# Kernel tuning notes

Measured on AMD Instinct MI355X. Metric: run time of the kernel, lower is better.

Reference implementation:

```python
import jax, jax.numpy as jnp
import numpy as np

N = 50000
IN_DIM = 256
HID = 64
HEADS = 4
OUT_DIM = 64
E = 800000
SLOPE = 0.2


def gat_conv(x, src, dst, W, a_src, a_dst, bias, heads, out_ch):
    """PyG-style GATConv: gather -> edge attention -> segment softmax -> scatter.
    x: [N, in], W: [in, heads*out_ch], a_src/a_dst: [heads, out_ch], bias: [heads*out_ch].
    Returns [N, heads*out_ch] (heads concatenated)."""
    n = x.shape[0]
    h = (x @ W).reshape(n, heads, out_ch)               # [N, H, C]
    s = jnp.einsum('nhc,hc->nh', h, a_src)              # [N, H]
    d = jnp.einsum('nhc,hc->nh', h, a_dst)              # [N, H]
    e = jax.nn.leaky_relu(s[src] + d[dst], SLOPE)       # [E, H]
    emax = jax.ops.segment_max(e, dst, num_segments=n)  # stable softmax per dst
    ex = jnp.exp(e - emax[dst])
    denom = jax.ops.segment_sum(ex, dst, num_segments=n)
    alpha = ex / (denom[dst] + 1e-16)                   # [E, H]
    msg = h[src] * alpha[:, :, None]                    # [E, H, C]
    out = jax.ops.segment_sum(msg, dst, num_segments=n) # [N, H, C]
    return out.reshape(n, heads * out_ch) + bias


def setup_inputs() -> dict:
    key = jax.random.key(0)
    ks = jax.random.split(key, 12)
    x = jax.random.normal(ks[0], (N, IN_DIM), dtype=jnp.float32)
    edge_index = jax.random.randint(ks[1], (2, E), 0, N, dtype=jnp.int64)
    sc = 0.1
    params = {
        'W1': jax.random.normal(ks[2], (IN_DIM, HEADS * HID), dtype=jnp.float32) * sc,
        'a_src1': jax.random.normal(ks[3], (HEADS, HID), dtype=jnp.float32) * sc,
        'a_dst1': jax.random.normal(ks[4], (HEADS, HID), dtype=jnp.float32) * sc,
        'b1': jnp.zeros((HEADS * HID,), dtype=jnp.float32),
        'W2': jax.random.normal(ks[5], (HEADS * HID, HID), dtype=jnp.float32) * sc,
        'a_src2': jax.random.normal(ks[6], (1, HID), dtype=jnp.float32) * sc,
        'a_dst2': jax.random.normal(ks[7], (1, HID), dtype=jnp.float32) * sc,
        'b2': jnp.zeros((HID,), dtype=jnp.float32),
        'Wf1': jax.random.normal(ks[8], (HID, HID), dtype=jnp.float32) * sc,
        'bf1': jnp.zeros((HID,), dtype=jnp.float32),
        'Wf2': jax.random.normal(ks[9], (HID, OUT_DIM), dtype=jnp.float32) * sc,
        'bf2': jnp.zeros((OUT_DIM,), dtype=jnp.float32),
    }
    return {'x': x, 'edge_index': edge_index, **params}


def reference(x, edge_index, W1, a_src1, a_dst1, b1, W2, a_src2, a_dst2, b2,
              Wf1, bf1, Wf2, bf2):
    n = x.shape[0]
    # PyG GATConv adds self-loops by default
    loops = jnp.arange(n, dtype=edge_index.dtype)
    src = jnp.concatenate([edge_index[0], loops])
    dst = jnp.concatenate([edge_index[1], loops])
    h = jax.nn.relu(gat_conv(x, src, dst, W1, a_src1, a_dst1, b1, HEADS, HID))
    h = jax.nn.relu(gat_conv(h, src, dst, W2, a_src2, a_dst2, b2, 1, HID))
    h = jax.nn.relu(h @ Wf1 + bf1)
    return jax.nn.softmax(h @ Wf2 + bf2, axis=1)
```

## Files before the change

### kernel.cpp

```cpp
#include <hip/hip_runtime.h>

#define NNODES 50000
#define NEDGES 800000
#define INDIM  256
#define HIDC   64
#define HEADS  4
static constexpr int ETOT = NEDGES + NNODES;

typedef _Float16 half8 __attribute__((ext_vector_type(8)));
typedef short    s16x8 __attribute__((ext_vector_type(8)));
typedef short    s16x4 __attribute__((ext_vector_type(4)));
typedef float    f32x4 __attribute__((ext_vector_type(4)));

__device__ __forceinline__ unsigned short f2bf(float f) {
    unsigned u = __float_as_uint(f);
    u += 0x7fffu + ((u >> 16) & 1u);
    return (unsigned short)(u >> 16);
}
__device__ __forceinline__ float bf2f(unsigned short h) {
    return __uint_as_float(((unsigned)h) << 16);
}

__device__ __forceinline__ int is_int64(const unsigned* __restrict__ ei32) {
    int r = 1;
    #pragma unroll
    for (int i = 1; i < 64; i += 2) r &= (ei32[i] == 0u);
    return r;
}

__device__ __forceinline__ int load_idx(const void* ei, int is64, size_t pos) {
    return is64 ? (int)((const long long*)ei)[pos] : ((const int*)ei)[pos];
}

__global__ __launch_bounds__(256)
void hist_k(const void* __restrict__ ei, int* __restrict__ count) {
    int e = blockIdx.x * 256 + threadIdx.x;
    if (e >= ETOT) return;
    int is64 = is_int64((const unsigned*)ei);
    int dst = (e < NEDGES) ? load_idx(ei, is64, (size_t)NEDGES + e) : (e - NEDGES);
    atomicAdd(&count[dst], 1);
}

__global__ __launch_bounds__(1024)
void scan1_k(const int* __restrict__ count, int* __restrict__ rowptr,
             int* __restrict__ bsum, int n) {
    __shared__ int wsum[16];
    const int tid = threadIdx.x;
    const int lane = tid & 63;
    const int w = tid >> 6;
    int i = blockIdx.x * 1024 + tid;
    int v = (i < n) ? count[i] : 0;
    int x = v;
    #pragma unroll
    for (int dd = 1; dd < 64; dd <<= 1) {
        int y = __shfl_up(x, dd);
        if (lane >= dd) x += y;
    }
    if (lane == 63) wsum[w] = x;
    __syncthreads();
    int woff = 0, total = 0;
    #pragma unroll
    for (int j = 0; j < 16; ++j) {
        if (j < w) woff += wsum[j];
        total += wsum[j];
    }
    if (i < n) rowptr[i] = woff + x - v;
    if (tid == 0) bsum[blockIdx.x] = total;
}

__global__ void scan2_k(int* __restrict__ bsum, int* __restrict__ bpre, int nb,
                        int* __restrict__ rowptr, int n) {
    int lane = threadIdx.x;
    int v = (lane < nb) ? bsum[lane] : 0;
    int x = v;
    #pragma unroll
    for (int dd = 1; dd < 64; dd <<= 1) {
        int y = __shfl_up(x, dd);
        if (lane >= dd) x += y;
    }
    if (lane < nb) bpre[lane] = x - v;
    if (lane == 63) rowptr[n] = x;
}

__global__ __launch_bounds__(1024)
void scan3_k(int* __restrict__ rowptr, const int* __restrict__ bpre, int n) {
    int i = blockIdx.x * 1024 + threadIdx.x;
    if (i < n) rowptr[i] += bpre[blockIdx.x];
}

__global__ __launch_bounds__(256)
void scatter_k(const void* __restrict__ ei, const int* __restrict__ rowptr,
               int* __restrict__ fill, int* __restrict__ csr_src) {
    int e = blockIdx.x * 256 + threadIdx.x;
    if (e >= ETOT) return;
    int is64 = is_int64((const unsigned*)ei);
    int src, dst;
    if (e < NEDGES) {
        src = load_idx(ei, is64, (size_t)e);
        dst = load_idx(ei, is64, (size_t)NEDGES + e);
    } else {
        src = e - NEDGES; dst = src;
    }
    int pos = rowptr[dst] + atomicAdd(&fill[dst], 1);
    csr_src[pos] = src;
}

__global__ __launch_bounds__(256)
void convall_k(const float* __restrict__ W1, const float* __restrict__ W2,
               const float* __restrict__ Wf1, const float* __restrict__ Wf2,
               unsigned short* __restrict__ w1h, unsigned short* __restrict__ w1l,
               unsigned short* __restrict__ w2h, unsigned short* __restrict__ w2l,
               unsigned short* __restrict__ f1h, unsigned short* __restrict__ f1l,
               unsigned short* __restrict__ f2h, unsigned short* __restrict__ f2l) {
    int idx = blockIdx.x * 256 + threadIdx.x;
    const float* W; unsigned short *th, *tl; int K, N;
    if (idx < 65536)       { W = W1;  th = w1h; tl = w1l; K = 256; N = 256; }
    else if (idx < 81920)  { idx -= 65536; W = W2;  th = w2h; tl = w2l; K = 256; N = 64; }
    else if (idx < 86016)  { idx -= 81920; W = Wf1; th = f1h; tl = f1l; K = 64;  N = 64; }
    else if (idx < 90112)  { idx -= 86016; W = Wf2; th = f2h; tl = f2l; K = 64;  N = 64; }
    else return;
    int k = idx / N, n = idx % N;
    float w = W[(size_t)k * N + n];
    unsigned short hi = f2bf(w);
    unsigned short lo = f2bf(w - bf2f(hi));
    th[(size_t)n * K + k] = hi;
    tl[(size_t)n * K + k] = lo;
}

template<int BN, int SD>
__global__ __launch_bounds__(256)
void gemm_mfma_k(const float* __restrict__ A,
                 const unsigned short* __restrict__ Bt_hi,
                 const unsigned short* __restrict__ Bt_lo,
                 _Float16* __restrict__ Ch,
                 const float* __restrict__ asrc, const float* __restrict__ adst,
                 float* __restrict__ S, float* __restrict__ D,
                 int M, int N, int K) {
    constexpr int CB = BN / 32;
    constexpr int BI = (BN * 4) / 256;
    __shared__ unsigned short sAh[128][40], sAl[128][40];
    __shared__ unsigned short sBh[BN][40], sBl[BN][40];
    const int tid = threadIdx.x;
    const int bm = blockIdx.y * 128;
    const int bn = blockIdx.x * BN;
    const int w = tid >> 6, lane = tid & 63;
    const int wr = w >> 1, wc = w & 1;
    const int lr = lane & 15, lk = lane >> 4;

    f32x4 acc[4][CB] = {};

    for (int k0 = 0; k0 < K; k0 += 32) {
        float4 av[4];
        #pragma unroll
        for (int i = 0; i < 4; ++i) {
            int idx = tid + 256 * i;
            int row = idx >> 3, c4 = idx & 7;
            int grow = bm + row; if (grow >= M) grow = M - 1;
            av[i] = *(const float4*)(A + (size_t)grow * K + k0 + c4 * 4);
        }
        s16x8 bhv[BI], blv[BI];
        #pragma unroll
        for (int i = 0; i < BI; ++i) {
            int idx = tid + 256 * i;
            int col = idx >> 2, ch = idx & 3;
            bhv[i] = *(const s16x8*)(Bt_hi + (size_t)(bn + col) * K + k0 + ch * 8);
            blv[i] = *(const s16x8*)(Bt_lo + (size_t)(bn + col) * K + k0 + ch * 8);
        }
        __syncthreads();
        #pragma unroll
        for (int i = 0; i < 4; ++i) {
            int idx = tid + 256 * i;
            int row = idx >> 3, c4 = idx & 7;
            float vs[4] = {av[i].x, av[i].y, av[i].z, av[i].w};
            unsigned short h[4], l[4];
            #pragma unroll
            for (int j = 0; j < 4; ++j) {
                h[j] = f2bf(vs[j]);
                l[j] = f2bf(vs[j] - bf2f(h[j]));
            }
            *(s16x4*)&sAh[row][c4 * 4] = (s16x4){(short)h[0], (short)h[1], (short)h[2], (short)h[3]};
            *(s16x4*)&sAl[row][c4 * 4] = (s16x4){(short)l[0], (short)l[1], (short)l[2], (short)l[3]};
        }
        #pragma unroll
        for (int i = 0; i < BI; ++i) {
            int idx = tid + 256 * i;
            int col = idx >> 2, ch = idx & 3;
            *(s16x8*)&sBh[col][ch * 8] = bhv[i];
            *(s16x8*)&sBl[col][ch * 8] = blv[i];
        }
        __syncthreads();
        s16x8 afh[4], afl[4], bfh[CB], bfl[CB];
        #pragma unroll
        for (int rb = 0; rb < 4; ++rb) {
            int row = wr * 64 + rb * 16 + lr;
            afh[rb] = *(const s16x8*)&sAh[row][lk * 8];
            afl[rb] = *(const s16x8*)&sAl[row][lk * 8];
        }
        #pragma unroll
        for (int cb = 0; cb < CB; ++cb) {
            int col = wc * (BN / 2) + cb * 16 + lr;
            bfh[cb] = *(const s16x8*)&sBh[col][lk * 8];
            bfl[cb] = *(const s16x8*)&sBl[col][lk * 8];
        }
        #pragma unroll
        for (int rb = 0; rb < 4; ++rb)
            #pragma unroll
            for (int cb = 0; cb < CB; ++cb) {
                acc[rb][cb] = __builtin_amdgcn_mfma_f32_16x16x32_bf16(afh[rb], bfh[cb], acc[rb][cb], 0, 0, 0);
                acc[rb][cb] = __builtin_amdgcn_mfma_f32_16x16x32_bf16(afh[rb], bfl[cb], acc[rb][cb], 0, 0, 0);
                acc[rb][cb] = __builtin_amdgcn_mfma_f32_16x16x32_bf16(afl[rb], bfh[cb], acc[rb][cb], 0, 0, 0);
            }
    }
    #pragma unroll
    for (int rb = 0; rb < 4; ++rb)
        #pragma unroll
        for (int cb = 0; cb < CB; ++cb)
            #pragma unroll
            for (int r = 0; r < 4; ++r) {
                int row = bm + wr * 64 + rb * 16 + lk * 4 + r;
                int col = bn + wc * (BN / 2) + cb * 16 + lr;
                if (row < M) Ch[(size_t)row * N + col] = (_Float16)acc[rb][cb][r];
            }
    {
        float af[CB], df[CB];
        #pragma unroll
        for (int cb = 0; cb < CB; ++cb) {
            int colg = bn + wc * (BN / 2) + cb * 16 + lr;
            af[cb] = asrc[colg];
            df[cb] = adst[colg];
        }
        #pragma unroll
        for (int rb = 0; rb < 4; ++rb)
            #pragma unroll
            for (int r = 0; r < 4; ++r) {
                float ps = 0.f, pd = 0.f;
                #pragma unroll
                for (int cb = 0; cb < CB; ++cb) {
                    ps += acc[rb][cb][r] * af[cb];
                    pd += acc[rb][cb][r] * df[cb];
                }
                #pragma unroll
                for (int m = 1; m < 16; m <<= 1) {
                    ps += __shfl_xor(ps, m);
                    pd += __shfl_xor(pd, m);
                }
                int row = bm + wr * 64 + rb * 16 + lk * 4 + r;
                if (lr == 0 && row < M) {
                    if constexpr (SD == 1) {
                        int head = (bn + wc * (BN / 2)) >> 6;
                        S[(size_t)row * (N >> 6) + head] = ps;
                        D[(size_t)row * (N >> 6) + head] = pd;
                    } else {
                        atomicAdd(&S[row], ps);
                        atomicAdd(&D[row], pd);
                    }
                }
            }
    }
}

__device__ __forceinline__ float leaky(float e) { return (e > 0.f) ? e : 0.2f * e; }

__device__ __forceinline__ float sel4(const float v[4], int idx) {
    float r = v[0];
    r = (idx == 1) ? v[1] : r;
    r = (idx == 2) ? v[2] : r;
    r = (idx == 3) ? v[3] : r;
    return r;
}

template<int H>
__global__ __launch_bounds__(256)
void agg_k(const _Float16* __restrict__ hhalf,
           const float* __restrict__ s, const float* __restrict__ d,
           const float* __restrict__ bias, const int* __restrict__ rowptr,
           const int* __restrict__ csr_src, float* __restrict__ out, int n) {
    __shared__ float exs[4][H][64];
    __shared__ int   srcs[4][64];
    const int lane = threadIdx.x & 63;
    const int wv   = threadIdx.x >> 6;
    const int node = blockIdx.x * 4 + wv;
    if (node >= n) return;
    const int beg = rowptr[node], end = rowptr[node + 1];
    float dh[H], dn[H];
    #pragma unroll
    for (int h = 0; h < H; ++h) { dh[h] = d[node * H + h]; dn[h] = 0.f; }
    const half8* H8 = (const half8*)hhalf;

    if constexpr (H == 4) {
        const int sub = lane >> 5, c8 = lane & 31, head = c8 >> 3;
        float acc[8] = {};
        for (int c0 = beg; c0 < end; c0 += 64) {
            const int cend = (c0 + 64 < end) ? c0 + 64 : end;
            int e = c0 + lane;
            if (e < end) {
                int sidx = csr_src[e];
                float4 sv = *(const float4*)(s + (size_t)sidx * 4);
                float e0 = __expf(leaky(sv.x + dh[0]));
                float e1 = __expf(leaky(sv.y + dh[1]));
                float e2 = __expf(leaky(sv.z + dh[2]));
                float e3 = __expf(leaky(sv.w + dh[3]));
                srcs[wv][lane] = sidx;
                exs[wv][0][lane] = e0; exs[wv][1][lane] = e1;
                exs[wv][2][lane] = e2; exs[wv][3][lane] = e3;
                dn[0] += e0; dn[1] += e1; dn[2] += e2; dn[3] += e3;
            }
            asm volatile("s_waitcnt lgkmcnt(0)" ::: "memory");
            int i = c0;
            for (; i + 7 < cend; i += 8) {
                int j = i - c0 + sub;
                int s0 = srcs[wv][j],     s1 = srcs[wv][j + 2];
                int s2 = srcs[wv][j + 4], s3 = srcs[wv][j + 6];
                float x0 = exs[wv][head][j],     x1 = exs[wv][head][j + 2];
                float x2 = exs[wv][head][j + 4], x3 = exs[wv][head][j + 6];
                half8 h0 = H8[(size_t)s0 * 32 + c8];
                half8 h1 = H8[(size_t)s1 * 32 + c8];
                half8 h2 = H8[(size_t)s2 * 32 + c8];
                half8 h3 = H8[(size_t)s3 * 32 + c8];
                #pragma unroll
                for (int q = 0; q < 8; ++q)
                    acc[q] += x0 * (float)h0[q] + x1 * (float)h1[q]
                            + x2 * (float)h2[q] + x3 * (float)h3[q];
            }
            for (; i < cend; i += 2) {
                int e2i = i + sub;
                if (e2i < cend) {
                    int j = e2i - c0;
                    int s0 = srcs[wv][j];
                    float x = exs[wv][head][j];
                    half8 hh = H8[(size_t)s0 * 32 + c8];
                    #pragma unroll
                    for (int q = 0; q < 8; ++q) acc[q] += x * (float)hh[q];
                }
            }
        }
        float inv_[4];
        #pragma unroll
        for (int h = 0; h < 4; ++h) {
            #pragma unroll
            for (int m = 32; m; m >>= 1) dn[h] += __shfl_xor(dn[h], m);
            inv_[h] = 1.f / (dn[h] + 1e-16f);
        }
        const float invh = sel4(inv_, head);
        #pragma unroll
        for (int q = 0; q < 8; ++q) acc[q] += __shfl_xor(acc[q], 32);
        if (lane < 32) {
            float4 b0 = *(const float4*)(bias + c8 * 8);
            float4 b1 = *(const float4*)(bias + c8 * 8 + 4);
            float4 o0, o1;
            o0.x = fmaxf(acc[0] * invh + b0.x, 0.f);
            o0.y = fmaxf(acc[1] * invh + b0.y, 0.f);
            o0.z = fmaxf(acc[2] * invh + b0.z, 0.f);
            o0.w = fmaxf(acc[3] * invh + b0.w, 0.f);
            o1.x = fmaxf(acc[4] * invh + b1.x, 0.f);
            o1.y = fmaxf(acc[5] * invh + b1.y, 0.f);
            o1.z = fmaxf(acc[6] * invh + b1.z, 0.f);
            o1.w = fmaxf(acc[7] * invh + b1.w, 0.f);
            *(float4*)(out + (size_t)node * 256 + c8 * 8) = o0;
            *(float4*)(out + (size_t)node * 256 + c8 * 8 + 4) = o1;
        }
    } else {
        const int sub = lane >> 3, c8 = lane & 7;
        float acc[8] = {};
        for (int c0 = beg; c0 < end; c0 += 64) {
            const int cend = (c0 + 64 < end) ? c0 + 64 : end;
            int e = c0 + lane;
            if (e < end) {
                int sidx = csr_src[e];
                float ex = __expf(leaky(s[sidx] + dh[0]));
                srcs[wv][lane] = sidx;
                exs[wv][0][lane] = ex;
                dn[0] += ex;
            }
            asm volatile("s_waitcnt lgkmcnt(0)" ::: "memory");
            int i = c0;
            for (; i + 15 < cend; i += 16) {
                int j = i - c0 + sub;
                int s0 = srcs[wv][j], s1 = srcs[wv][j + 8];
                float x0 = exs[wv][0][j], x1 = exs[wv][0][j + 8];
                half8 h0 = H8[(size_t)s0 * 8 + c8];
                half8 h1 = H8[(size_t)s1 * 8 + c8];
                #pragma unroll
                for (int q = 0; q < 8; ++q)
                    acc[q] += x0 * (float)h0[q] + x1 * (float)h1[q];
            }
            for (; i < cend; i += 8) {
                int e2i = i + sub;
                if (e2i < cend) {
                    int j = e2i - c0;
                    int s0 = srcs[wv][j];
                    float x = exs[wv][0][j];
                    half8 hh = H8[(size_t)s0 * 8 + c8];
                    #pragma unroll
                    for (int q = 0; q < 8; ++q) acc[q] += x * (float)hh[q];
                }
            }
        }
        #pragma unroll
        for (int m = 32; m; m >>= 1) dn[0] += __shfl_xor(dn[0], m);
        const float inv0 = 1.f / (dn[0] + 1e-16f);
        #pragma unroll
        for (int m = 8; m <= 32; m <<= 1)
            #pragma unroll
            for (int q = 0; q < 8; ++q) acc[q] += __shfl_xor(acc[q], m);
        if (lane < 8) {
            float4 b0 = *(const float4*)(bias + c8 * 8);
            float4 b1 = *(const float4*)(bias + c8 * 8 + 4);
            float4 o0, o1;
            o0.x = fmaxf(acc[0] * inv0 + b0.x, 0.f);
            o0.y = fmaxf(acc[1] * inv0 + b0.y, 0.f);
            o0.z = fmaxf(acc[2] * inv0 + b0.z, 0.f);
            o0.w = fmaxf(acc[3] * inv0 + b0.w, 0.f);
            o1.x = fmaxf(acc[4] * inv0 + b1.x, 0.f);
            o1.y = fmaxf(acc[5] * inv0 + b1.y, 0.f);
            o1.z = fmaxf(acc[6] * inv0 + b1.z, 0.f);
            o1.w = fmaxf(acc[7] * inv0 + b1.w, 0.f);
            *(float4*)(out + (size_t)node * 64 + c8 * 8) = o0;
            *(float4*)(out + (size_t)node * 64 + c8 * 8 + 4) = o1;
        }
    }
}

__global__ __launch_bounds__(256)
void ffm_k(const float* __restrict__ in,
           const unsigned short* __restrict__ w1h, const unsigned short* __restrict__ w1l,
           const float* __restrict__ bf1,
           const unsigned short* __restrict__ w2h, const unsigned short* __restrict__ w2l,
           const float* __restrict__ bf2, float* __restrict__ out, int M) {
    __shared__ unsigned short sAh[64][80], sAl[64][80];
    __shared__ unsigned short sW1h[64][80], sW1l[64][80];
    __shared__ unsigned short sW2h[64][80], sW2l[64][80];
    const int tid = threadIdx.x;
    const int bm = blockIdx.x * 64;
    const int w = tid >> 6, lane = tid & 63;
    const int lr = lane & 15, lk = lane >> 4;

    for (int c = tid; c < 512; c += 256) {
        int n = c >> 3, k8 = c & 7;
        int dcol = (k8 >> 2) * 40 + (k8 & 3) * 8;
        *(s16x8*)&sW1h[n][dcol] = *(const s16x8*)(w1h + n * 64 + k8 * 8);
        *(s16x8*)&sW1l[n][dcol] = *(const s16x8*)(w1l + n * 64 + k8 * 8);
        *(s16x8*)&sW2h[n][dcol] = *(const s16x8*)(w2h + n * 64 + k8 * 8);
        *(s16x8*)&sW2l[n][dcol] = *(const s16x8*)(w2l + n * 64 + k8 * 8);
    }
    #pragma unroll
    for (int i = 0; i < 4; ++i) {
        int c = tid + 256 * i;
        int row = c >> 4, c4 = c & 15;
        int grow = bm + row; if (grow >= M) grow = M - 1;
        float4 av = *(const float4*)(in + (size_t)grow * 64 + c4 * 4);
        float vs[4] = {av.x, av.y, av.z, av.w};
        unsigned short h[4], l[4];
        #pragma unroll
        for (int j = 0; j < 4; ++j) {
            h[j] = f2bf(vs[j]);
            l[j] = f2bf(vs[j] - bf2f(h[j]));
        }
        int dcol = (c4 >> 3) * 40 + (c4 & 7) * 4;
        *(s16x4*)&sAh[row][dcol] = (s16x4){(short)h[0], (short)h[1], (short)h[2], (short)h[3]};
        *(s16x4*)&sAl[row][dcol] = (s16x4){(short)l[0], (short)l[1], (short)l[2], (short)l[3]};
    }
    __syncthreads();
    f32x4 a1[4] = {};
    #pragma unroll
    for (int ks = 0; ks < 2; ++ks) {
        int koff = ks * 40 + lk * 8;
        s16x8 ah = *(const s16x8*)&sAh[w * 16 + lr][koff];
        s16x8 al = *(const s16x8*)&sAl[w * 16 + lr][koff];
        #pragma unroll
        for (int cb = 0; cb < 4; ++cb) {
            s16x8 bh = *(const s16x8*)&sW1h[cb * 16 + lr][koff];
            s16x8 bl = *(const s16x8*)&sW1l[cb * 16 + lr][koff];
            a1[cb] = __builtin_amdgcn_mfma_f32_16x16x32_bf16(ah, bh, a1[cb], 0, 0, 0);
            a1[cb] = __builtin_amdgcn_mfma_f32_16x16x32_bf16(ah, bl, a1[cb], 0, 0, 0);
            a1[cb] = __builtin_amdgcn_mfma_f32_16x16x32_bf16(al, bh, a1[cb], 0, 0, 0);
        }
    }
    __syncthreads();
    #pragma unroll
    for (int cb = 0; cb < 4; ++cb) {
        int col = cb * 16 + lr;
        float b = bf1[col];
        int dcol = (col >> 5) * 40 + (col & 31);
        #pragma unroll
        for (int r = 0; r < 4; ++r) {
            int row = w * 16 + lk * 4 + r;
            float y = fmaxf(a1[cb][r] + b, 0.f);
            unsigned short hh = f2bf(y);
            sAh[row][dcol] = hh;
            sAl[row][dcol] = f2bf(y - bf2f(hh));
        }
    }
    __syncthreads();
    f32x4 a2[4] = {};
    #pragma unroll
    for (int ks = 0; ks < 2; ++ks) {
        int koff = ks * 40 + lk * 8;
        s16x8 ah = *(const s16x8*)&sAh[w * 16 + lr][koff];
        s16x8 al = *(const s16x8*)&sAl[w * 16 + lr][koff];
        #pragma unroll
        for (int cb = 0; cb < 4; ++cb) {
            s16x8 bh = *(const s16x8*)&sW2h[cb * 16 + lr][koff];
            s16x8 bl = *(const s16x8*)&sW2l[cb * 16 + lr][koff];
            a2[cb] = __builtin_amdgcn_mfma_f32_16x16x32_bf16(ah, bh, a2[cb], 0, 0, 0);
            a2[cb] = __builtin_amdgcn_mfma_f32_16x16x32_bf16(ah, bl, a2[cb], 0, 0, 0);
            a2[cb] = __builtin_amdgcn_mfma_f32_16x16x32_bf16(al, bh, a2[cb], 0, 0, 0);
        }
    }
    float zb[4];
    #pragma unroll
    for (int cb = 0; cb < 4; ++cb) zb[cb] = bf2[cb * 16 + lr];
    #pragma unroll
    for (int r = 0; r < 4; ++r) {
        int row = bm + w * 16 + lk * 4 + r;
        float z0 = a2[0][r] + zb[0], z1 = a2[1][r] + zb[1];
        float z2 = a2[2][r] + zb[2], z3 = a2[3][r] + zb[3];
        float m = fmaxf(fmaxf(z0, z1), fmaxf(z2, z3));
        #pragma unroll
        for (int dd = 1; dd < 16; dd <<= 1) m = fmaxf(m, __shfl_xor(m, dd));
        float e0 = __expf(z0 - m), e1 = __expf(z1 - m);
        float e2 = __expf(z2 - m), e3 = __expf(z3 - m);
        float sum = e0 + e1 + e2 + e3;
        #pragma unroll
        for (int dd = 1; dd < 16; dd <<= 1) sum += __shfl_xor(sum, dd);
        float is = 1.f / sum;
        if (row < M) {
            out[(size_t)row * 64 + 0 + lr]  = e0 * is;
            out[(size_t)row * 64 + 16 + lr] = e1 * is;
            out[(size_t)row * 64 + 32 + lr] = e2 * is;
            out[(size_t)row * 64 + 48 + lr] = e3 * is;
        }
    }
}

extern "C" void kernel_launch(void* const* d_in, const int* in_sizes, int n_in,
                              void* d_out, int out_size, void* d_ws, size_t ws_size,
                              hipStream_t stream) {
    const float* x      = (const float*)d_in[0];
    const void*  ei     = d_in[1];
    const float* W1     = (const float*)d_in[2];
    const float* a_src1 = (const float*)d_in[3];
    const float* a_dst1 = (const float*)d_in[4];
    const float* b1     = (const float*)d_in[5];
    const float* W2     = (const float*)d_in[6];
    const float* a_src2 = (const float*)d_in[7];
    const float* a_dst2 = (const float*)d_in[8];
    const float* b2     = (const float*)d_in[9];
    const float* Wf1    = (const float*)d_in[10];
    const float* bf1    = (const float*)d_in[11];
    const float* Wf2    = (const float*)d_in[12];
    const float* bf2    = (const float*)d_in[13];
    float* outp = (float*)d_out;

    char* ws = (char*)d_ws;
    size_t off = 0;
    auto take = [&](size_t bytes) -> char* {
        char* p = ws + off;
        off += (bytes + 255) & ~(size_t)255;
        return p;
    };
    int*   count  = (int*)take((size_t)NNODES * 4);
    int*   fill   = (int*)take((size_t)NNODES * 4);
    int*   rowptr = (int*)take((size_t)(NNODES + 1) * 4);
    int*   bsum   = (int*)take(64 * 4);
    int*   bpre   = (int*)take(64 * 4);
    int*   csr    = (int*)take((size_t)ETOT * 4);
    unsigned short* w1t_hi = (unsigned short*)take((size_t)256 * 256 * 2);
    unsigned short* w1t_lo = (unsigned short*)take((size_t)256 * 256 * 2);
    unsigned short* w2t_hi = (unsigned short*)take((size_t)64 * 256 * 2);
    unsigned short* w2t_lo = (unsigned short*)take((size_t)64 * 256 * 2);
    unsigned short* wf1t_hi = (unsigned short*)take((size_t)64 * 64 * 2);
    unsigned short* wf1t_lo = (unsigned short*)take((size_t)64 * 64 * 2);
    unsigned short* wf2t_hi = (unsigned short*)take((size_t)64 * 64 * 2);
    unsigned short* wf2t_lo = (unsigned short*)take((size_t)64 * 64 * 2);
    float* agg1   = (float*)take((size_t)NNODES * 256 * 4);
    float* s1     = (float*)take((size_t)NNODES * HEADS * 4);
    float* d1     = (float*)take((size_t)NNODES * HEADS * 4);
    _Float16* h1h = (_Float16*)take((size_t)NNODES * 256 * 2);
    float*    s2   = s1;
    float*    d2   = d1;
    float*    agg2 = agg1;
    _Float16* h2h  = h1h;

    hipMemsetAsync(count, 0, (size_t)((char*)fill - (char*)count) + (size_t)NNODES * 4, stream);
    const int eblocks = (ETOT + 255) / 256;
    hist_k<<<eblocks, 256, 0, stream>>>(ei, count);
    const int sblocks = (NNODES + 1023) / 1024;
    scan1_k<<<sblocks, 1024, 0, stream>>>(count, rowptr, bsum, NNODES);
    scan2_k<<<1, 64, 0, stream>>>(bsum, bpre, sblocks, rowptr, NNODES);
    scan3_k<<<sblocks, 1024, 0, stream>>>(rowptr, bpre, NNODES);
    scatter_k<<<eblocks, 256, 0, stream>>>(ei, rowptr, fill, csr);

    convall_k<<<(90112 + 255) / 256, 256, 0, stream>>>(
        W1, W2, Wf1, Wf2, w1t_hi, w1t_lo, w2t_hi, w2t_lo,
        wf1t_hi, wf1t_lo, wf2t_hi, wf2t_lo);

    const int nodeblocks = NNODES / 4;
    const int mblocks = (NNODES + 127) / 128;
    const dim3 gg1(2, mblocks);
    const dim3 gg2(1, mblocks);

    gemm_mfma_k<128, 1><<<gg1, 256, 0, stream>>>(x, w1t_hi, w1t_lo,
        h1h, a_src1, a_dst1, s1, d1, NNODES, 256, 256);
    agg_k<HEADS><<<nodeblocks, 256, 0, stream>>>(h1h, s1, d1, b1,
        rowptr, csr, agg1, NNODES);

    hipMemsetAsync(s2, 0, (size_t)((char*)d1 - (char*)s1) + (size_t)NNODES * 4, stream);
    gemm_mfma_k<64, 2><<<gg2, 256, 0, stream>>>(agg1, w2t_hi, w2t_lo,
        h2h, a_src2, a_dst2, s2, d2, NNODES, 64, 256);
    agg_k<1><<<nodeblocks, 256, 0, stream>>>(h2h, s2, d2, b2,
        rowptr, csr, agg2, NNODES);

    ffm_k<<<(NNODES + 63) / 64, 256, 0, stream>>>(agg2, wf1t_hi, wf1t_lo,
        bf1, wf2t_hi, wf2t_lo, bf2, outp, NNODES);
}
```

Before: 280.3 us.

## Store layer-1 aggregate in fp16, merge scan kernels, drop atomics for layer-2 scores

The layer-1 aggregation now writes its ReLU output as fp16 instead of fp32, and the second GEMM is templated to read fp16 A directly, which halves that intermediate's write and read traffic. The two scan tail kernels are merged into one that recomputes block prefixes per block with wave reductions. Layer-2 attention scores are combined across the two column warps through shared memory and written directly, which removes the atomics and the memset before them. The fp16 intermediate adds rounding error on the hidden activations.

```diff
diff --git a/kernel.cpp b/kernel.cpp
--- a/kernel.cpp
+++ b/kernel.cpp
@@ -68,24 +68,25 @@
     if (tid == 0) bsum[blockIdx.x] = total;
 }
 
-__global__ void scan2_k(int* __restrict__ bsum, int* __restrict__ bpre, int nb,
-                        int* __restrict__ rowptr, int n) {
-    int lane = threadIdx.x;
-    int v = (lane < nb) ? bsum[lane] : 0;
-    int x = v;
-    #pragma unroll
-    for (int dd = 1; dd < 64; dd <<= 1) {
-        int y = __shfl_up(x, dd);
-        if (lane >= dd) x += y;
-    }
-    if (lane < nb) bpre[lane] = x - v;
-    if (lane == 63) rowptr[n] = x;
-}
-
 __global__ __launch_bounds__(1024)
-void scan3_k(int* __restrict__ rowptr, const int* __restrict__ bpre, int n) {
-    int i = blockIdx.x * 1024 + threadIdx.x;
-    if (i < n) rowptr[i] += bpre[blockIdx.x];
+void scan3_k(int* __restrict__ rowptr, const int* __restrict__ bsum,
+             int nb, int n) {
+    __shared__ int spre, stot;
+    const int tid = threadIdx.x;
+    if (tid < 64) {
+        int vall = (tid < nb) ? bsum[tid] : 0;
+        int vpre = (tid < (int)blockIdx.x) ? vall : 0;
+        #pragma unroll
+        for (int m = 32; m; m >>= 1) {
+            vall += __shfl_xor(vall, m);
+            vpre += __shfl_xor(vpre, m);
+        }
+        if (tid == 0) { spre = vpre; stot = vall; }
+    }
+    __syncthreads();
+    int i = blockIdx.x * 1024 + tid;
+    if (i < n) rowptr[i] += spre;
+    if (blockIdx.x == 0 && tid == 0) rowptr[n] = stot;
 }
 
 __global__ __launch_bounds__(256)
@@ -127,9 +128,9 @@
     tl[(size_t)n * K + k] = lo;
 }
 
-template<int BN, int SD>
+template<int BN, int SD, typename AT>
 __global__ __launch_bounds__(256)
-void gemm_mfma_k(const float* __restrict__ A,
+void gemm_mfma_k(const AT* __restrict__ A,
                  const unsigned short* __restrict__ Bt_hi,
                  const unsigned short* __restrict__ Bt_lo,
                  _Float16* __restrict__ Ch,
@@ -151,12 +152,23 @@
 
     for (int k0 = 0; k0 < K; k0 += 32) {
         float4 av[4];
-        #pragma unroll
-        for (int i = 0; i < 4; ++i) {
-            int idx = tid + 256 * i;
-            int row = idx >> 3, c4 = idx & 7;
-            int grow = bm + row; if (grow >= M) grow = M - 1;
-            av[i] = *(const float4*)(A + (size_t)grow * K + k0 + c4 * 4);
+        half8 avh[2];
+        if constexpr (sizeof(AT) == 4) {
+            #pragma unroll
+            for (int i = 0; i < 4; ++i) {
+                int idx = tid + 256 * i;
+                int row = idx >> 3, c4 = idx & 7;
+                int grow = bm + row; if (grow >= M) grow = M - 1;
+                av[i] = *(const float4*)((const float*)A + (size_t)grow * K + k0 + c4 * 4);
+            }
+        } else {
+            #pragma unroll
+            for (int i = 0; i < 2; ++i) {
+                int idx = tid + 256 * i;
+                int row = idx >> 2, c8 = idx & 3;
+                int grow = bm + row; if (grow >= M) grow = M - 1;
+                avh[i] = *(const half8*)((const _Float16*)A + (size_t)grow * K + k0 + c8 * 8);
+            }
         }
         s16x8 bhv[BI], blv[BI];
         #pragma unroll
@@ -167,19 +179,38 @@
             blv[i] = *(const s16x8*)(Bt_lo + (size_t)(bn + col) * K + k0 + ch * 8);
         }
         __syncthreads();
-        #pragma unroll
-        for (int i = 0; i < 4; ++i) {
-            int idx = tid + 256 * i;
-            int row = idx >> 3, c4 = idx & 7;
-            float vs[4] = {av[i].x, av[i].y, av[i].z, av[i].w};
-            unsigned short h[4], l[4];
-            #pragma unroll
-            for (int j = 0; j < 4; ++j) {
-                h[j] = f2bf(vs[j]);
-                l[j] = f2bf(vs[j] - bf2f(h[j]));
-            }
-            *(s16x4*)&sAh[row][c4 * 4] = (s16x4){(short)h[0], (short)h[1], (short)h[2], (short)h[3]};
-            *(s16x4*)&sAl[row][c4 * 4] = (s16x4){(short)l[0], (short)l[1], (short)l[2], (short)l[3]};
+        if constexpr (sizeof(AT) == 4) {
+            #pragma unroll
+            for (int i = 0; i < 4; ++i) {
+                int idx = tid + 256 * i;
+                int row = idx >> 3, c4 = idx & 7;
+                float vs[4] = {av[i].x, av[i].y, av[i].z, av[i].w};
+                unsigned short h[4], l[4];
+                #pragma unroll
+                for (int j = 0; j < 4; ++j) {
+                    h[j] = f2bf(vs[j]);
+                    l[j] = f2bf(vs[j] - bf2f(h[j]));
+                }
+                *(s16x4*)&sAh[row][c4 * 4] = (s16x4){(short)h[0], (short)h[1], (short)h[2], (short)h[3]};
+                *(s16x4*)&sAl[row][c4 * 4] = (s16x4){(short)l[0], (short)l[1], (short)l[2], (short)l[3]};
+            }
+        } else {
+            #pragma unroll
+            for (int i = 0; i < 2; ++i) {
+                int idx = tid + 256 * i;
+                int row = idx >> 2, c8 = idx & 3;
+                unsigned short h[8], l[8];
+                #pragma unroll
+                for (int j = 0; j < 8; ++j) {
+                    float v = (float)avh[i][j];
+                    h[j] = f2bf(v);
+                    l[j] = f2bf(v - bf2f(h[j]));
+                }
+                *(s16x8*)&sAh[row][c8 * 8] = (s16x8){(short)h[0], (short)h[1], (short)h[2], (short)h[3],
+                                                     (short)h[4], (short)h[5], (short)h[6], (short)h[7]};
+                *(s16x8*)&sAl[row][c8 * 8] = (s16x8){(short)l[0], (short)l[1], (short)l[2], (short)l[3],
+                                                     (short)l[4], (short)l[5], (short)l[6], (short)l[7]};
+            }
         }
         #pragma unroll
         for (int i = 0; i < BI; ++i) {
@@ -229,6 +260,7 @@
             af[cb] = asrc[colg];
             df[cb] = adst[colg];
         }
+        float psA[4][4], pdA[4][4];
         #pragma unroll
         for (int rb = 0; rb < 4; ++rb)
             #pragma unroll
@@ -244,18 +276,46 @@
                     ps += __shfl_xor(ps, m);
                     pd += __shfl_xor(pd, m);
                 }
-                int row = bm + wr * 64 + rb * 16 + lk * 4 + r;
-                if (lr == 0 && row < M) {
-                    if constexpr (SD == 1) {
+                psA[rb][r] = ps; pdA[rb][r] = pd;
+            }
+        if constexpr (SD == 1) {
+            #pragma unroll
+            for (int rb = 0; rb < 4; ++rb)
+                #pragma unroll
+                for (int r = 0; r < 4; ++r) {
+                    int row = bm + wr * 64 + rb * 16 + lk * 4 + r;
+                    if (lr == 0 && row < M) {
                         int head = (bn + wc * (BN / 2)) >> 6;
-                        S[(size_t)row * (N >> 6) + head] = ps;
-                        D[(size_t)row * (N >> 6) + head] = pd;
-                    } else {
-                        atomicAdd(&S[row], ps);
-                        atomicAdd(&D[row], pd);
+                        S[(size_t)row * (N >> 6) + head] = psA[rb][r];
+                        D[(size_t)row * (N >> 6) + head] = pdA[rb][r];
                     }
                 }
-            }
+        } else {
+            __shared__ float sps[128], spd[128];
+            if (wc == 1 && lr == 0) {
+                #pragma unroll
+                for (int rb = 0; rb < 4; ++rb)
+                    #pragma unroll
+                    for (int r = 0; r < 4; ++r) {
+                        int rowb = wr * 64 + rb * 16 + lk * 4 + r;
+                        sps[rowb] = psA[rb][r]; spd[rowb] = pdA[rb][r];
+                    }
+            }
+            __syncthreads();
+            if (wc == 0 && lr == 0) {
+                #pragma unroll
+                for (int rb = 0; rb < 4; ++rb)
+                    #pragma unroll
+                    for (int r = 0; r < 4; ++r) {
+                        int rowb = wr * 64 + rb * 16 + lk * 4 + r;
+                        int row = bm + rowb;
+                        if (row < M) {
+                            S[row] = psA[rb][r] + sps[rowb];
+                            D[row] = pdA[rb][r] + spd[rowb];
+                        }
+                    }
+            }
+        }
     }
 }
 
@@ -274,7 +334,8 @@
 void agg_k(const _Float16* __restrict__ hhalf,
            const float* __restrict__ s, const float* __restrict__ d,
            const float* __restrict__ bias, const int* __restrict__ rowptr,
-           const int* __restrict__ csr_src, float* __restrict__ out, int n) {
+           const int* __restrict__ csr_src, _Float16* __restrict__ outh,
+           float* __restrict__ outf, int n) {
     __shared__ float exs[4][H][64];
     __shared__ int   srcs[4][64];
     const int lane = threadIdx.x & 63;
@@ -347,17 +408,12 @@
         if (lane < 32) {
             float4 b0 = *(const float4*)(bias + c8 * 8);
             float4 b1 = *(const float4*)(bias + c8 * 8 + 4);
-            float4 o0, o1;
-            o0.x = fmaxf(acc[0] * invh + b0.x, 0.f);
-            o0.y = fmaxf(acc[1] * invh + b0.y, 0.f);
-            o0.z = fmaxf(acc[2] * invh + b0.z, 0.f);
-            o0.w = fmaxf(acc[3] * invh + b0.w, 0.f);
-            o1.x = fmaxf(acc[4] * invh + b1.x, 0.f);
-            o1.y = fmaxf(acc[5] * invh + b1.y, 0.f);
-            o1.z = fmaxf(acc[6] * invh + b1.z, 0.f);
-            o1.w = fmaxf(acc[7] * invh + b1.w, 0.f);
-            *(float4*)(out + (size_t)node * 256 + c8 * 8) = o0;
-            *(float4*)(out + (size_t)node * 256 + c8 * 8 + 4) = o1;
+            float bb[8] = {b0.x, b0.y, b0.z, b0.w, b1.x, b1.y, b1.z, b1.w};
+            half8 o;
+            #pragma unroll
+            for (int q = 0; q < 8; ++q)
+                o[q] = (_Float16)fmaxf(acc[q] * invh + bb[q], 0.f);
+            *(half8*)(outh + (size_t)node * 256 + c8 * 8) = o;
         }
     } else {
         const int sub = lane >> 3, c8 = lane & 7;
@@ -415,8 +471,8 @@
             o1.y = fmaxf(acc[5] * inv0 + b1.y, 0.f);
             o1.z = fmaxf(acc[6] * inv0 + b1.z, 0.f);
             o1.w = fmaxf(acc[7] * inv0 + b1.w, 0.f);
-            *(float4*)(out + (size_t)node * 64 + c8 * 8) = o0;
-            *(float4*)(out + (size_t)node * 64 + c8 * 8 + 4) = o1;
+            *(float4*)(outf + (size_t)node * 64 + c8 * 8) = o0;
+            *(float4*)(outf + (size_t)node * 64 + c8 * 8 + 4) = o1;
         }
     }
 }
@@ -563,7 +619,6 @@
     int*   fill   = (int*)take((size_t)NNODES * 4);
     int*   rowptr = (int*)take((size_t)(NNODES + 1) * 4);
     int*   bsum   = (int*)take(64 * 4);
-    int*   bpre   = (int*)take(64 * 4);
     int*   csr    = (int*)take((size_t)ETOT * 4);
     unsigned short* w1t_hi = (unsigned short*)take((size_t)256 * 256 * 2);
     unsigned short* w1t_lo = (unsigned short*)take((size_t)256 * 256 * 2);
@@ -573,22 +628,21 @@
     unsigned short* wf1t_lo = (unsigned short*)take((size_t)64 * 64 * 2);
     unsigned short* wf2t_hi = (unsigned short*)take((size_t)64 * 64 * 2);
     unsigned short* wf2t_lo = (unsigned short*)take((size_t)64 * 64 * 2);
-    float* agg1   = (float*)take((size_t)NNODES * 256 * 4);
+    float* agg2   = (float*)take((size_t)NNODES * 64 * 4);
     float* s1     = (float*)take((size_t)NNODES * HEADS * 4);
     float* d1     = (float*)take((size_t)NNODES * HEADS * 4);
-    _Float16* h1h = (_Float16*)take((size_t)NNODES * 256 * 2);
-    float*    s2   = s1;
-    float*    d2   = d1;
-    float*    agg2 = agg1;
-    _Float16* h2h  = h1h;
+    _Float16* h1h   = (_Float16*)take((size_t)NNODES * 256 * 2);
+    _Float16* agg1h = (_Float16*)take((size_t)NNODES * 256 * 2);
+    float*    s2  = s1;
+    float*    d2  = d1;
+    _Float16* h2h = h1h;
 
     hipMemsetAsync(count, 0, (size_t)((char*)fill - (char*)count) + (size_t)NNODES * 4, stream);
     const int eblocks = (ETOT + 255) / 256;
     hist_k<<<eblocks, 256, 0, stream>>>(ei, count);
     const int sblocks = (NNODES + 1023) / 1024;
     scan1_k<<<sblocks, 1024, 0, stream>>>(count, rowptr, bsum, NNODES);
-    scan2_k<<<1, 64, 0, stream>>>(bsum, bpre, sblocks, rowptr, NNODES);
-    scan3_k<<<sblocks, 1024, 0, stream>>>(rowptr, bpre, NNODES);
+    scan3_k<<<sblocks, 1024, 0, stream>>>(rowptr, bsum, sblocks, NNODES);
     scatter_k<<<eblocks, 256, 0, stream>>>(ei, rowptr, fill, csr);
 
     convall_k<<<(90112 + 255) / 256, 256, 0, stream>>>(
@@ -600,16 +654,15 @@
     const dim3 gg1(2, mblocks);
     const dim3 gg2(1, mblocks);
 
-    gemm_mfma_k<128, 1><<<gg1, 256, 0, stream>>>(x, w1t_hi, w1t_lo,
+    gemm_mfma_k<128, 1, float><<<gg1, 256, 0, stream>>>(x, w1t_hi, w1t_lo,
         h1h, a_src1, a_dst1, s1, d1, NNODES, 256, 256);
     agg_k<HEADS><<<nodeblocks, 256, 0, stream>>>(h1h, s1, d1, b1,
-        rowptr, csr, agg1, NNODES);
-
-    hipMemsetAsync(s2, 0, (size_t)((char*)d1 - (char*)s1) + (size_t)NNODES * 4, stream);
-    gemm_mfma_k<64, 2><<<gg2, 256, 0, stream>>>(agg1, w2t_hi, w2t_lo,
+        rowptr, csr, agg1h, nullptr, NNODES);
+
+    gemm_mfma_k<64, 2, _Float16><<<gg2, 256, 0, stream>>>(agg1h, w2t_hi, w2t_lo,
         h2h, a_src2, a_dst2, s2, d2, NNODES, 64, 256);
     agg_k<1><<<nodeblocks, 256, 0, stream>>>(h2h, s2, d2, b2,
-        rowptr, csr, agg2, NNODES);
+        rowptr, csr, nullptr, agg2, NNODES);
 
     ffm_k<<<(NNODES + 63) / 64, 256, 0, stream>>>(agg2, wf1t_hi, wf1t_lo,
         bf1, wf2t_hi, wf2t_lo, bf2, outp, NNODES);
```

Result: faster. 273.9 us (-2.3%).
